# Kernel optimization log

Hardware: AMD Instinct MI355X
Metric: run time of the kernel (lower is better)

The kernel has to match this reference:

```python
import jax, jax.numpy as jnp
import numpy as np

NUM_EXPERTS = 8
EXPERTS_PER_TOK = 2

def setup_inputs() -> dict:
    key = jax.random.key(0)
    k1, k2, k3, k4, k5 = jax.random.split(key, 5)
    B, T, D, F, E = 4, 1024, 2048, 1024, NUM_EXPERTS
    return {
        "x": jax.random.normal(k1, (B, T, D), dtype=jnp.float32),
        "router_w": jax.random.normal(k2, (D, E), dtype=jnp.float32) * 0.02,
        "gate_proj": jax.random.normal(k3, (E, D, F), dtype=jnp.float32) * 0.02,
        "up_proj": jax.random.normal(k4, (E, D, F), dtype=jnp.float32) * 0.02,
        "down_proj": jax.random.normal(k5, (E, F, D), dtype=jnp.float32) * 0.02,
    }

def reference(x, router_w, gate_proj, up_proj, down_proj):
    E, K = NUM_EXPERTS, EXPERTS_PER_TOK
    # Router: softmax over experts, take top-k, renormalize.
    scores = jnp.einsum('btd,de->bte', x, router_w).astype(jnp.float32)
    routing_weights, routing_idx = jax.lax.top_k(jax.nn.softmax(scores, axis=-1), K)
    routing_weights = (routing_weights / jnp.sum(routing_weights, axis=-1, keepdims=True)).astype(x.dtype)
    # one_hot: [B,T,K,E]. Sum over K gives 0/1 dispatch mask [B,T,E]
    # (top-k indices are distinct). Weighted sum gives combine weights.
    onehot = jax.nn.one_hot(routing_idx, E, dtype=x.dtype)
    dispatch_mask = jnp.sum(onehot, axis=2)                      # [B,T,E]
    combine_weights = jnp.einsum('btke,btk->bte', onehot, routing_weights)
    # Dense masked dispatch (same math as original einsum with size-1 I axis).
    dispatched = x[:, :, None, :] * dispatch_mask[..., None]     # [B,T,E,D]
    # SwiGLU FFN for every expert, batched over E.
    gate = jnp.einsum('bted,edf->btef', dispatched, gate_proj)
    up = jnp.einsum('bted,edf->btef', dispatched, up_proj)
    act = jax.nn.silu(gate) * up                                 # [B,T,E,F]
    expert_out = jnp.einsum('btef,efd->bted', act, down_proj)    # [B,T,E,D]
    # Combine: weights already include the dispatch mask via one-hot.
    return jnp.einsum('bted,bte->btd', expert_out, combine_weights)
```

## Files before the change

### kernel.cpp

```cpp
#include <hip/hip_runtime.h>
#include <stdint.h>

#define BT 4096
#define DMODEL 2048
#define FDIM 1024
#define NEXP 8
#define NA (BT * 2)
#define MAXTILES 72

typedef __attribute__((ext_vector_type(8))) __bf16 bf16x8;
typedef __attribute__((ext_vector_type(4))) float f32x4;

#define FENCE() asm volatile("" ::: "memory")
#define BARRIER() do { FENCE(); __builtin_amdgcn_s_barrier(); FENCE(); } while (0)
#define VMCNT0()  asm volatile("s_waitcnt vmcnt(0)" ::: "memory")

__device__ __forceinline__ unsigned short f2bf(float f) {
  union { float f; unsigned int u; } v; v.f = f;
  unsigned int u = v.u;
  unsigned int r = (u + 0x7fffu + ((u >> 16) & 1u)) >> 16;
  return (unsigned short)r;
}

__device__ __forceinline__ void g2l16(const void* g, void* l) {
  __builtin_amdgcn_global_load_lds((const __attribute__((address_space(1))) void*)g,
                                   (__attribute__((address_space(3))) void*)l, 16, 0, 0);
}


__global__ void k_router(const float* __restrict__ x, const float* __restrict__ rw,
                         unsigned short* __restrict__ xbf,
                         int* __restrict__ tok_e, float* __restrict__ tok_w) {
  int wid = threadIdx.x >> 6;
  int lane = threadIdx.x & 63;
  int t = blockIdx.x * 4 + wid;
  float acc[8];
#pragma unroll
  for (int e = 0; e < 8; e++) acc[e] = 0.0f;
  const float* xr = x + (size_t)t * DMODEL;
  unsigned short* xbr = xbf + (size_t)t * DMODEL;
#pragma unroll
  for (int d0 = lane * 4; d0 < DMODEL; d0 += 256) {
    float4 xv = *(const float4*)(xr + d0);
    ushort4 o = make_ushort4(f2bf(xv.x), f2bf(xv.y), f2bf(xv.z), f2bf(xv.w));
    *(ushort4*)(xbr + d0) = o;
    const float* xs = &xv.x;
#pragma unroll
    for (int j = 0; j < 4; j++) {
      const float4* r4 = (const float4*)(rw + (size_t)(d0 + j) * NEXP);
      float4 ra = r4[0], rb = r4[1];
      float xj = xs[j];
      acc[0] += xj * ra.x; acc[1] += xj * ra.y; acc[2] += xj * ra.z; acc[3] += xj * ra.w;
      acc[4] += xj * rb.x; acc[5] += xj * rb.y; acc[6] += xj * rb.z; acc[7] += xj * rb.w;
    }
  }
#pragma unroll
  for (int e = 0; e < 8; e++) {
    float v = acc[e];
#pragma unroll
    for (int off = 32; off > 0; off >>= 1) v += __shfl_xor(v, off);
    acc[e] = v;
  }
  if (lane == 0) {
    int e0 = 0; float s0 = acc[0];
#pragma unroll
    for (int e = 1; e < 8; e++) if (acc[e] > s0) { s0 = acc[e]; e0 = e; }
    int e1 = (e0 == 0) ? 1 : 0; float s1 = acc[e1];
#pragma unroll
    for (int e = 0; e < 8; e++) if (e != e0 && acc[e] > s1) { s1 = acc[e]; e1 = e; }
    float w0 = 1.0f / (1.0f + __expf(s1 - s0));
    tok_e[t * 2] = e0; tok_e[t * 2 + 1] = e1;
    tok_w[t * 2] = w0; tok_w[t * 2 + 1] = 1.0f - w0;
  }
}

__global__ void k_scanbuild(const int* __restrict__ tok_e, int* __restrict__ offsets,
                            int* __restrict__ tile_e, int* __restrict__ tile_y,
                            int* __restrict__ ntiles, int* __restrict__ cursors) {
  __shared__ int hist[NEXP];
  int tid = threadIdx.x;
  if (tid < NEXP) hist[tid] = 0;
  __syncthreads();
  for (int i = tid; i < NA; i += 256) atomicAdd(&hist[tok_e[i]], 1);
  __syncthreads();
  if (tid == 0) {
    int s = 0;
    for (int e = 0; e < NEXP; e++) { offsets[e] = s; s += hist[e]; }
    offsets[NEXP] = s;
    int idx = 0;
    for (int e = 0; e < NEXP; e++) {
      int nt = (hist[e] + 127) >> 7;
      for (int y = 0; y < nt; y++) { tile_e[idx] = e; tile_y[idx] = y; idx++; }
    }
    *ntiles = idx;
    for (int i = idx; i < MAXTILES; i++) { tile_e[i] = 0; tile_y[i] = 0; }
  }
  if (tid < NEXP) cursors[tid] = 0;
}

__global__ void k_scatter(const int* __restrict__ tok_e, const float* __restrict__ tok_w,
                          const int* __restrict__ offsets, int* __restrict__ cursors,
                          int* __restrict__ assign_token, float* __restrict__ assign_w) {
  int i = blockIdx.x * 256 + threadIdx.x;
  if (i >= NA) return;
  int e = tok_e[i];
  int pos = offsets[e] + atomicAdd(&cursors[e], 1);
  assign_token[pos] = i >> 1;
  assign_w[pos] = tok_w[i];
}

__global__ void k_transpose_all(const float* __restrict__ gw, const float* __restrict__ uw,
                                const float* __restrict__ dw,
                                unsigned short* __restrict__ wtgu,
                                unsigned short* __restrict__ wtd) {
  __shared__ float tile[64][65];
  int z = blockIdx.y;
  const float* src; unsigned short* dst; int N, Kd;
  if (z < 8)       { src = gw + (size_t)z * DMODEL * FDIM;        dst = wtgu + (size_t)z * 2 * FDIM * DMODEL;        N = FDIM;   Kd = DMODEL; }
  else if (z < 16) { src = uw + (size_t)(z - 8) * DMODEL * FDIM;  dst = wtgu + (size_t)(z - 8) * 2 * FDIM * DMODEL;  N = FDIM;   Kd = DMODEL; }
  else             { src = dw + (size_t)(z - 16) * FDIM * DMODEL; dst = wtd + (size_t)(z - 16) * FDIM * DMODEL;      N = DMODEL; Kd = FDIM; }
  int ntx = N >> 6;
  int bx = blockIdx.x;
  int n0 = (bx % ntx) * 64, k0 = (bx / ntx) * 64;
  int rr = threadIdx.x >> 4, cc = threadIdx.x & 15;
#pragma unroll
  for (int i = 0; i < 4; i++) {
    int k = rr + i * 16;
    float4 v = *(const float4*)(src + (size_t)(k0 + k) * N + n0 + cc * 4);
    tile[k][cc * 4 + 0] = v.x; tile[k][cc * 4 + 1] = v.y;
    tile[k][cc * 4 + 2] = v.z; tile[k][cc * 4 + 3] = v.w;
  }
  __syncthreads();
#pragma unroll
  for (int i = 0; i < 4; i++) {
    int n = rr + i * 16;
    int gr = n0 + n;
    int orow;
    if (z < 8)       orow = ((gr & ~31) << 1) + (gr & 31);
    else if (z < 16) orow = ((gr & ~31) << 1) + 32 + (gr & 31);
    else             orow = gr;
    ushort4 o = make_ushort4(f2bf(tile[cc * 4 + 0][n]), f2bf(tile[cc * 4 + 1][n]),
                             f2bf(tile[cc * 4 + 2][n]), f2bf(tile[cc * 4 + 3][n]));
    *(ushort4*)(dst + (size_t)orow * Kd + k0 + cc * 4) = o;
  }
}


__global__ __launch_bounds__(256, 2) void k_gemm1(
    const unsigned short* __restrict__ xbf,
    const unsigned short* __restrict__ wtgu,
    const int* __restrict__ offsets,
    const int* __restrict__ tile_e, const int* __restrict__ tile_y,
    const int* __restrict__ ntiles,
    const int* __restrict__ assign_token,
    unsigned short* __restrict__ act) {
  const int ti = blockIdx.y;
  if (ti >= *ntiles) return;
  const int e = tile_e[ti];
  const int row_beg = offsets[e], row_end = offsets[e + 1];
  const int m_base = row_beg + tile_y[ti] * 128;
  const int n_base = blockIdx.x * 128;

  __shared__ unsigned short As[2][128][64];
  __shared__ unsigned short Bs[2][128][64];

  const int tid = threadIdx.x;
  const int lane = tid & 63, wid = tid >> 6;
  const int wr = wid >> 1, wc = wid & 1;
  const int srow = wid * 8 + (lane >> 3);
  const int scol_d = (lane & 7) * 8;
  const int scol_s = ((lane & 7) ^ (lane >> 3)) * 8;
  const int sw = (lane & 7) * 8;

  const unsigned short* wb = wtgu + (size_t)e * 2 * FDIM * DMODEL + (size_t)n_base * DMODEL;

  size_t arow[4];
#pragma unroll
  for (int i = 0; i < 4; i++) {
    int slot = m_base + i * 32 + srow;
    if (slot >= row_end) slot = row_end - 1;
    arow[i] = (size_t)assign_token[slot] * DMODEL;
  }

  f32x4 acc[4][4];
#pragma unroll
  for (int m = 0; m < 4; m++)
#pragma unroll
    for (int n = 0; n < 4; n++) acc[m][n] = f32x4{0.f, 0.f, 0.f, 0.f};

  auto stage = [&](int buf, int k0) {
#pragma unroll
    for (int i = 0; i < 4; i++)
      g2l16(xbf + arow[i] + k0 + scol_s, &As[buf][i * 32 + srow][scol_d]);
#pragma unroll
    for (int i = 0; i < 4; i++)
      g2l16(wb + (size_t)(i * 32 + srow) * DMODEL + k0 + scol_s, &Bs[buf][i * 32 + srow][scol_d]);
  };

  const int NT = DMODEL / 64;
  stage(0, 0);
  VMCNT0(); BARRIER();

  for (int t = 0; t < NT; ++t) {
    const int cur = t & 1, nxt = cur ^ 1;
    if (t + 1 < NT) stage(nxt, (t + 1) * 64);
#pragma unroll
    for (int kk = 0; kk < 2; kk++) {
      const int ko = kk * 32 + (lane >> 4) * 8;
      bf16x8 a[4], b[4];
#pragma unroll
      for (int m = 0; m < 4; m++)
        a[m] = *(const bf16x8*)&As[cur][wr * 64 + m * 16 + (lane & 15)][ko ^ sw];
#pragma unroll
      for (int n = 0; n < 4; n++)
        b[n] = *(const bf16x8*)&Bs[cur][wc * 64 + n * 16 + (lane & 15)][ko ^ sw];
      __builtin_amdgcn_s_setprio(1);
#pragma unroll
      for (int m = 0; m < 4; m++)
#pragma unroll
        for (int n = 0; n < 4; n++)
          acc[m][n] = __builtin_amdgcn_mfma_f32_16x16x32_bf16(a[m], b[n], acc[m][n], 0, 0, 0);
      __builtin_amdgcn_s_setprio(0);
    }
    VMCNT0(); BARRIER();
  }

  const int cr = (lane >> 4) * 4;
  const int ccc = lane & 15;
#pragma unroll
  for (int m = 0; m < 4; m++) {
#pragma unroll
    for (int j = 0; j < 4; j++) {
      int slot = m_base + wr * 64 + m * 16 + cr + j;
      if (slot < row_end) {
        unsigned short* dst = act + (size_t)slot * FDIM + (n_base >> 1) + wc * 32 + ccc;
#pragma unroll
        for (int n = 0; n < 2; n++) {
          float g = acc[m][n][j], u = acc[m][n + 2][j];
          float h = (g / (1.0f + __expf(-g))) * u;
          dst[n * 16] = f2bf(h);
        }
      }
    }
  }
}


__global__ __launch_bounds__(256, 2) void k_gemm2(
    const unsigned short* __restrict__ act,
    const unsigned short* __restrict__ wtd,
    const int* __restrict__ offsets,
    const int* __restrict__ tile_e, const int* __restrict__ tile_y,
    const int* __restrict__ ntiles,
    const int* __restrict__ assign_token,
    const float* __restrict__ assign_w,
    float* __restrict__ out) {
  const int ti = blockIdx.y;
  if (ti >= *ntiles) return;
  const int e = tile_e[ti];
  const int row_beg = offsets[e], row_end = offsets[e + 1];
  const int m_base = row_beg + tile_y[ti] * 128;
  const int n_base = blockIdx.x * 128;

  __shared__ unsigned short As[2][128][64];
  __shared__ unsigned short Bs[2][128][64];

  const int tid = threadIdx.x;
  const int lane = tid & 63, wid = tid >> 6;
  const int wr = wid >> 1, wc = wid & 1;
  const int srow = wid * 8 + (lane >> 3);
  const int scol_d = (lane & 7) * 8;
  const int scol_s = ((lane & 7) ^ (lane >> 3)) * 8;
  const int sw = (lane & 7) * 8;

  const unsigned short* wd_e = wtd + (size_t)e * DMODEL * FDIM + (size_t)n_base * FDIM;

  size_t arow[4];
#pragma unroll
  for (int i = 0; i < 4; i++) {
    int slot = m_base + i * 32 + srow;
    if (slot >= row_end) slot = row_end - 1;
    arow[i] = (size_t)slot * FDIM;
  }

  f32x4 acc[4][4];
#pragma unroll
  for (int m = 0; m < 4; m++)
#pragma unroll
    for (int n = 0; n < 4; n++) acc[m][n] = f32x4{0.f, 0.f, 0.f, 0.f};

  auto stage = [&](int buf, int k0) {
#pragma unroll
    for (int i = 0; i < 4; i++)
      g2l16(act + arow[i] + k0 + scol_s, &As[buf][i * 32 + srow][scol_d]);
#pragma unroll
    for (int i = 0; i < 4; i++)
      g2l16(wd_e + (size_t)(i * 32 + srow) * FDIM + k0 + scol_s, &Bs[buf][i * 32 + srow][scol_d]);
  };

  const int NT = FDIM / 64;
  stage(0, 0);
  VMCNT0(); BARRIER();

  for (int t = 0; t < NT; ++t) {
    const int cur = t & 1, nxt = cur ^ 1;
    if (t + 1 < NT) stage(nxt, (t + 1) * 64);
#pragma unroll
    for (int kk = 0; kk < 2; kk++) {
      const int ko = kk * 32 + (lane >> 4) * 8;
      bf16x8 a[4], b[4];
#pragma unroll
      for (int m = 0; m < 4; m++)
        a[m] = *(const bf16x8*)&As[cur][wr * 64 + m * 16 + (lane & 15)][ko ^ sw];
#pragma unroll
      for (int n = 0; n < 4; n++)
        b[n] = *(const bf16x8*)&Bs[cur][wc * 64 + n * 16 + (lane & 15)][ko ^ sw];
      __builtin_amdgcn_s_setprio(1);
#pragma unroll
      for (int m = 0; m < 4; m++)
#pragma unroll
        for (int n = 0; n < 4; n++)
          acc[m][n] = __builtin_amdgcn_mfma_f32_16x16x32_bf16(a[m], b[n], acc[m][n], 0, 0, 0);
      __builtin_amdgcn_s_setprio(0);
    }
    VMCNT0(); BARRIER();
  }

  const int cr = (lane >> 4) * 4;
  const int ccc = lane & 15;
#pragma unroll
  for (int m = 0; m < 4; m++) {
#pragma unroll
    for (int j = 0; j < 4; j++) {
      int slot = m_base + wr * 64 + m * 16 + cr + j;
      if (slot < row_end) {
        int tok = assign_token[slot];
        float w = assign_w[slot];
        float* dst = out + (size_t)tok * DMODEL + n_base + wc * 64 + ccc;
#pragma unroll
        for (int n = 0; n < 4; n++)
          atomicAdd(&dst[n * 16], acc[m][n][j] * w);
      }
    }
  }
}


extern "C" void kernel_launch(void* const* d_in, const int* in_sizes, int n_in,
                              void* d_out, int out_size, void* d_ws, size_t ws_size,
                              hipStream_t stream) {
  const float* x  = (const float*)d_in[0];
  const float* rw = (const float*)d_in[1];
  const float* gw = (const float*)d_in[2];
  const float* uw = (const float*)d_in[3];
  const float* dw = (const float*)d_in[4];
  float* out = (float*)d_out;

  char* ws = (char*)d_ws;
  size_t off = 0;
  auto alloc = [&](size_t bytes) {
    size_t o = off;
    off += (bytes + 255) & ~(size_t)255;
    return o;
  };
  unsigned short* xbf    = (unsigned short*)(ws + alloc((size_t)BT * DMODEL * 2));
  unsigned short* wtgu   = (unsigned short*)(ws + alloc((size_t)NEXP * 2 * FDIM * DMODEL * 2));
  unsigned short* wtd    = (unsigned short*)(ws + alloc((size_t)NEXP * DMODEL * FDIM * 2));
  unsigned short* act    = (unsigned short*)(ws + alloc((size_t)NA * FDIM * 2));
  int*   offsets = (int*)(ws + alloc((NEXP + 1) * 4));
  int*   cursors = (int*)(ws + alloc(NEXP * 4));
  int*   tok_e   = (int*)(ws + alloc(NA * 4));
  float* tok_w   = (float*)(ws + alloc(NA * 4));
  int*   assign_token = (int*)(ws + alloc(NA * 4));
  float* assign_w     = (float*)(ws + alloc(NA * 4));
  int*   tile_e       = (int*)(ws + alloc(MAXTILES * 4));
  int*   tile_y       = (int*)(ws + alloc(MAXTILES * 4));
  int*   ntiles       = (int*)(ws + alloc(4));
  if (off > ws_size) return;

  hipMemsetAsync(out, 0, (size_t)out_size * 4, stream);
  k_router<<<BT / 4, 256, 0, stream>>>(x, rw, xbf, tok_e, tok_w);
  k_scanbuild<<<1, 256, 0, stream>>>(tok_e, offsets, tile_e, tile_y, ntiles, cursors);
  k_scatter<<<NA / 256, 256, 0, stream>>>(tok_e, tok_w, offsets, cursors,
                                          assign_token, assign_w);
  k_transpose_all<<<dim3(512, 24), 256, 0, stream>>>(gw, uw, dw, wtgu, wtd);
  k_gemm1<<<dim3(DMODEL / 128, MAXTILES), 256, 0, stream>>>(xbf, wtgu, offsets,
                                                            tile_e, tile_y, ntiles,
                                                            assign_token, act);
  k_gemm2<<<dim3(DMODEL / 128, MAXTILES), 256, 0, stream>>>(act, wtd, offsets,
                                                            tile_e, tile_y, ntiles,
                                                            assign_token, assign_w, out);
}
```

Measured before the change: 340.8 us.

## Enlarge expert GEMM M-tiles to 256 rows and drop LDS double buffering

Both grouped expert GEMMs now use 256-row M tiles (each wave computes 128x64 with an 8x4 MFMA accumulator grid), so there are fewer tiles and each weight tile fetched from memory is reused across twice as many token rows. To fit the larger A tile in LDS, the double-buffered async staging is replaced by a single buffer with __syncthreads before and after each load. That removes the overlap between global loads and MFMA work. It also doubles accumulator register pressure and gives more padding waste on the partial last tile of each expert.

```diff
diff --git a/kernel.cpp b/kernel.cpp
--- a/kernel.cpp
+++ b/kernel.cpp
@@ -6,14 +6,10 @@
 #define FDIM 1024
 #define NEXP 8
 #define NA (BT * 2)
-#define MAXTILES 72
+#define MAXT 40
 
 typedef __attribute__((ext_vector_type(8))) __bf16 bf16x8;
 typedef __attribute__((ext_vector_type(4))) float f32x4;
-
-#define FENCE() asm volatile("" ::: "memory")
-#define BARRIER() do { FENCE(); __builtin_amdgcn_s_barrier(); FENCE(); } while (0)
-#define VMCNT0()  asm volatile("s_waitcnt vmcnt(0)" ::: "memory")
 
 __device__ __forceinline__ unsigned short f2bf(float f) {
   union { float f; unsigned int u; } v; v.f = f;
@@ -89,11 +85,11 @@
     offsets[NEXP] = s;
     int idx = 0;
     for (int e = 0; e < NEXP; e++) {
-      int nt = (hist[e] + 127) >> 7;
+      int nt = (hist[e] + 255) >> 8;
       for (int y = 0; y < nt; y++) { tile_e[idx] = e; tile_y[idx] = y; idx++; }
     }
     *ntiles = idx;
-    for (int i = idx; i < MAXTILES; i++) { tile_e[i] = 0; tile_y[i] = 0; }
+    for (int i = idx; i < MAXT; i++) { tile_e[i] = 0; tile_y[i] = 0; }
   }
   if (tid < NEXP) cursors[tid] = 0;
 }
@@ -158,82 +154,75 @@
   if (ti >= *ntiles) return;
   const int e = tile_e[ti];
   const int row_beg = offsets[e], row_end = offsets[e + 1];
-  const int m_base = row_beg + tile_y[ti] * 128;
+  const int m_base = row_beg + tile_y[ti] * 256;
   const int n_base = blockIdx.x * 128;
 
-  __shared__ unsigned short As[2][128][64];
-  __shared__ unsigned short Bs[2][128][64];
+  __shared__ unsigned short As[256][64];
+  __shared__ unsigned short Bs[128][64];
 
   const int tid = threadIdx.x;
   const int lane = tid & 63, wid = tid >> 6;
-  const int wr = wid >> 1, wc = wid & 1;
-  const int srow = wid * 8 + (lane >> 3);
-  const int scol_d = (lane & 7) * 8;
-  const int scol_s = ((lane & 7) ^ (lane >> 3)) * 8;
+  const int wm = wid >> 1, wn = wid & 1;
+  const int l15 = lane & 15;
+  const int srow = tid >> 3;
+  const int scol_d = (tid & 7) * 8;
+  const int scol_s = ((tid & 7) ^ (srow & 7)) * 8;
   const int sw = (lane & 7) * 8;
 
   const unsigned short* wb = wtgu + (size_t)e * 2 * FDIM * DMODEL + (size_t)n_base * DMODEL;
 
-  size_t arow[4];
-#pragma unroll
-  for (int i = 0; i < 4; i++) {
+  int arow8[8];
+#pragma unroll
+  for (int i = 0; i < 8; i++) {
     int slot = m_base + i * 32 + srow;
     if (slot >= row_end) slot = row_end - 1;
-    arow[i] = (size_t)assign_token[slot] * DMODEL;
-  }
-
-  f32x4 acc[4][4];
-#pragma unroll
-  for (int m = 0; m < 4; m++)
+    arow8[i] = assign_token[slot] * DMODEL;
+  }
+
+  f32x4 acc[8][4];
+#pragma unroll
+  for (int m = 0; m < 8; m++)
 #pragma unroll
     for (int n = 0; n < 4; n++) acc[m][n] = f32x4{0.f, 0.f, 0.f, 0.f};
 
-  auto stage = [&](int buf, int k0) {
+  for (int k0 = 0; k0 < DMODEL; k0 += 64) {
+    __syncthreads();
+#pragma unroll
+    for (int i = 0; i < 8; i++)
+      g2l16(xbf + arow8[i] + k0 + scol_s, &As[i * 32 + srow][scol_d]);
 #pragma unroll
     for (int i = 0; i < 4; i++)
-      g2l16(xbf + arow[i] + k0 + scol_s, &As[buf][i * 32 + srow][scol_d]);
-#pragma unroll
-    for (int i = 0; i < 4; i++)
-      g2l16(wb + (size_t)(i * 32 + srow) * DMODEL + k0 + scol_s, &Bs[buf][i * 32 + srow][scol_d]);
-  };
-
-  const int NT = DMODEL / 64;
-  stage(0, 0);
-  VMCNT0(); BARRIER();
-
-  for (int t = 0; t < NT; ++t) {
-    const int cur = t & 1, nxt = cur ^ 1;
-    if (t + 1 < NT) stage(nxt, (t + 1) * 64);
+      g2l16(wb + (size_t)(i * 32 + srow) * DMODEL + k0 + scol_s, &Bs[i * 32 + srow][scol_d]);
+    __syncthreads();
+
 #pragma unroll
     for (int kk = 0; kk < 2; kk++) {
       const int ko = kk * 32 + (lane >> 4) * 8;
-      bf16x8 a[4], b[4];
-#pragma unroll
-      for (int m = 0; m < 4; m++)
-        a[m] = *(const bf16x8*)&As[cur][wr * 64 + m * 16 + (lane & 15)][ko ^ sw];
+      bf16x8 a[8], b[4];
+#pragma unroll
+      for (int m = 0; m < 8; m++)
+        a[m] = *(const bf16x8*)&As[wm * 128 + m * 16 + l15][ko ^ sw];
 #pragma unroll
       for (int n = 0; n < 4; n++)
-        b[n] = *(const bf16x8*)&Bs[cur][wc * 64 + n * 16 + (lane & 15)][ko ^ sw];
+        b[n] = *(const bf16x8*)&Bs[wn * 64 + n * 16 + l15][ko ^ sw];
       __builtin_amdgcn_s_setprio(1);
 #pragma unroll
-      for (int m = 0; m < 4; m++)
+      for (int m = 0; m < 8; m++)
 #pragma unroll
         for (int n = 0; n < 4; n++)
           acc[m][n] = __builtin_amdgcn_mfma_f32_16x16x32_bf16(a[m], b[n], acc[m][n], 0, 0, 0);
       __builtin_amdgcn_s_setprio(0);
     }
-    VMCNT0(); BARRIER();
   }
 
   const int cr = (lane >> 4) * 4;
-  const int ccc = lane & 15;
-#pragma unroll
-  for (int m = 0; m < 4; m++) {
+#pragma unroll
+  for (int m = 0; m < 8; m++) {
 #pragma unroll
     for (int j = 0; j < 4; j++) {
-      int slot = m_base + wr * 64 + m * 16 + cr + j;
+      int slot = m_base + wm * 128 + m * 16 + cr + j;
       if (slot < row_end) {
-        unsigned short* dst = act + (size_t)slot * FDIM + (n_base >> 1) + wc * 32 + ccc;
+        unsigned short* dst = act + (size_t)slot * FDIM + (n_base >> 1) + wn * 32 + l15;
 #pragma unroll
         for (int n = 0; n < 2; n++) {
           float g = acc[m][n][j], u = acc[m][n + 2][j];
@@ -259,84 +248,77 @@
   if (ti >= *ntiles) return;
   const int e = tile_e[ti];
   const int row_beg = offsets[e], row_end = offsets[e + 1];
-  const int m_base = row_beg + tile_y[ti] * 128;
+  const int m_base = row_beg + tile_y[ti] * 256;
   const int n_base = blockIdx.x * 128;
 
-  __shared__ unsigned short As[2][128][64];
-  __shared__ unsigned short Bs[2][128][64];
+  __shared__ unsigned short As[256][64];
+  __shared__ unsigned short Bs[128][64];
 
   const int tid = threadIdx.x;
   const int lane = tid & 63, wid = tid >> 6;
-  const int wr = wid >> 1, wc = wid & 1;
-  const int srow = wid * 8 + (lane >> 3);
-  const int scol_d = (lane & 7) * 8;
-  const int scol_s = ((lane & 7) ^ (lane >> 3)) * 8;
+  const int wm = wid >> 1, wn = wid & 1;
+  const int l15 = lane & 15;
+  const int srow = tid >> 3;
+  const int scol_d = (tid & 7) * 8;
+  const int scol_s = ((tid & 7) ^ (srow & 7)) * 8;
   const int sw = (lane & 7) * 8;
 
   const unsigned short* wd_e = wtd + (size_t)e * DMODEL * FDIM + (size_t)n_base * FDIM;
 
-  size_t arow[4];
-#pragma unroll
-  for (int i = 0; i < 4; i++) {
+  int arow8[8];
+#pragma unroll
+  for (int i = 0; i < 8; i++) {
     int slot = m_base + i * 32 + srow;
     if (slot >= row_end) slot = row_end - 1;
-    arow[i] = (size_t)slot * FDIM;
-  }
-
-  f32x4 acc[4][4];
-#pragma unroll
-  for (int m = 0; m < 4; m++)
+    arow8[i] = slot * FDIM;
+  }
+
+  f32x4 acc[8][4];
+#pragma unroll
+  for (int m = 0; m < 8; m++)
 #pragma unroll
     for (int n = 0; n < 4; n++) acc[m][n] = f32x4{0.f, 0.f, 0.f, 0.f};
 
-  auto stage = [&](int buf, int k0) {
+  for (int k0 = 0; k0 < FDIM; k0 += 64) {
+    __syncthreads();
+#pragma unroll
+    for (int i = 0; i < 8; i++)
+      g2l16(act + arow8[i] + k0 + scol_s, &As[i * 32 + srow][scol_d]);
 #pragma unroll
     for (int i = 0; i < 4; i++)
-      g2l16(act + arow[i] + k0 + scol_s, &As[buf][i * 32 + srow][scol_d]);
-#pragma unroll
-    for (int i = 0; i < 4; i++)
-      g2l16(wd_e + (size_t)(i * 32 + srow) * FDIM + k0 + scol_s, &Bs[buf][i * 32 + srow][scol_d]);
-  };
-
-  const int NT = FDIM / 64;
-  stage(0, 0);
-  VMCNT0(); BARRIER();
-
-  for (int t = 0; t < NT; ++t) {
-    const int cur = t & 1, nxt = cur ^ 1;
-    if (t + 1 < NT) stage(nxt, (t + 1) * 64);
+      g2l16(wd_e + (size_t)(i * 32 + srow) * FDIM + k0 + scol_s, &Bs[i * 32 + srow][scol_d]);
+    __syncthreads();
+
 #pragma unroll
     for (int kk = 0; kk < 2; kk++) {
       const int ko = kk * 32 + (lane >> 4) * 8;
-      bf16x8 a[4], b[4];
-#pragma unroll
-      for (int m = 0; m < 4; m++)
-        a[m] = *(const bf16x8*)&As[cur][wr * 64 + m * 16 + (lane & 15)][ko ^ sw];
+      bf16x8 a[8], b[4];
+#pragma unroll
+      for (int m = 0; m < 8; m++)
+        a[m] = *(const bf16x8*)&As[wm * 128 + m * 16 + l15][ko ^ sw];
 #pragma unroll
       for (int n = 0; n < 4; n++)
-        b[n] = *(const bf16x8*)&Bs[cur][wc * 64 + n * 16 + (lane & 15)][ko ^ sw];
+        b[n] = *(const bf16x8*)&Bs[wn * 64 + n * 16 + l15][ko ^ sw];
       __builtin_amdgcn_s_setprio(1);
 #pragma unroll
-      for (int m = 0; m < 4; m++)
+      for (int m = 0; m < 8; m++)
 #pragma unroll
         for (int n = 0; n < 4; n++)
           acc[m][n] = __builtin_amdgcn_mfma_f32_16x16x32_bf16(a[m], b[n], acc[m][n], 0, 0, 0);
       __builtin_amdgcn_s_setprio(0);
     }
-    VMCNT0(); BARRIER();
   }
 
   const int cr = (lane >> 4) * 4;
-  const int ccc = lane & 15;
-#pragma unroll
-  for (int m = 0; m < 4; m++) {
+#pragma unroll
+  for (int m = 0; m < 8; m++) {
 #pragma unroll
     for (int j = 0; j < 4; j++) {
-      int slot = m_base + wr * 64 + m * 16 + cr + j;
+      int slot = m_base + wm * 128 + m * 16 + cr + j;
       if (slot < row_end) {
         int tok = assign_token[slot];
         float w = assign_w[slot];
-        float* dst = out + (size_t)tok * DMODEL + n_base + wc * 64 + ccc;
+        float* dst = out + (size_t)tok * DMODEL + n_base + wn * 64 + l15;
 #pragma unroll
         for (int n = 0; n < 4; n++)
           atomicAdd(&dst[n * 16], acc[m][n][j] * w);
@@ -373,8 +355,8 @@
   float* tok_w   = (float*)(ws + alloc(NA * 4));
   int*   assign_token = (int*)(ws + alloc(NA * 4));
   float* assign_w     = (float*)(ws + alloc(NA * 4));
-  int*   tile_e       = (int*)(ws + alloc(MAXTILES * 4));
-  int*   tile_y       = (int*)(ws + alloc(MAXTILES * 4));
+  int*   tile_e       = (int*)(ws + alloc(MAXT * 4));
+  int*   tile_y       = (int*)(ws + alloc(MAXT * 4));
   int*   ntiles       = (int*)(ws + alloc(4));
   if (off > ws_size) return;
 
@@ -384,10 +366,10 @@
   k_scatter<<<NA / 256, 256, 0, stream>>>(tok_e, tok_w, offsets, cursors,
                                           assign_token, assign_w);
   k_transpose_all<<<dim3(512, 24), 256, 0, stream>>>(gw, uw, dw, wtgu, wtd);
-  k_gemm1<<<dim3(DMODEL / 128, MAXTILES), 256, 0, stream>>>(xbf, wtgu, offsets,
-                                                            tile_e, tile_y, ntiles,
-                                                            assign_token, act);
-  k_gemm2<<<dim3(DMODEL / 128, MAXTILES), 256, 0, stream>>>(act, wtd, offsets,
-                                                            tile_e, tile_y, ntiles,
-                                                            assign_token, assign_w, out);
-}
+  k_gemm1<<<dim3(2 * FDIM / 128, MAXT), 256, 0, stream>>>(xbf, wtgu, offsets,
+                                                          tile_e, tile_y, ntiles,
+                                                          assign_token, act);
+  k_gemm2<<<dim3(DMODEL / 128, MAXT), 256, 0, stream>>>(act, wtd, offsets,
+                                                        tile_e, tile_y, ntiles,
+                                                        assign_token, assign_w, out);
+}
```

After: 349.5 us. 2.6% more time.
